# Optimization experiments

Hardware: AMD Instinct MI355X
Metric: run time of the kernel (lower is better)

## Reference

```python
import jax, jax.numpy as jnp
import numpy as np

EMB = 256
HEAD = 8
D = 2 * EMB            # model dim = 512
HD = D // HEAD         # head dim = 64
SCALE = float(np.sqrt(D / HEAD))
NIT = 50               # entmax bisection iterations (entmax lib default)
LN_EPS = 1e-12


def _p(Z, am1):
    # [(alpha-1)x - tau]_+ ** (1/(alpha-1))
    return jnp.maximum(Z, 0.0) ** (1.0 / am1)


def _entmax_impl(X, alpha):
    # X: [B,H,L,L]; alpha: [B,H,L,1], alpha > 1. Faithful port of entmax_bisect.
    am1 = alpha - 1.0
    Xs = X * am1
    d = X.shape[-1]
    max_val = jnp.max(Xs, axis=-1, keepdims=True)
    tau_lo = max_val - 1.0                      # 1 ** (alpha-1)
    tau_hi = max_val - (1.0 / d) ** am1
    f_lo = jnp.sum(_p(Xs - tau_lo, am1), -1, keepdims=True) - 1.0
    dm0 = tau_hi - tau_lo

    def body(i, carry):
        tau_lo, dm, _ = carry
        dm = dm * 0.5
        tau_m = tau_lo + dm
        f_m = jnp.sum(_p(Xs - tau_m, am1), -1, keepdims=True) - 1.0
        tau_lo = jnp.where(f_m * f_lo >= 0, tau_m, tau_lo)
        return (tau_lo, dm, tau_m)

    _, _, tau_m = jax.lax.fori_loop(0, NIT, body, (tau_lo, dm0, tau_lo))
    p = _p(Xs - tau_m, am1)
    return p / jnp.sum(p, -1, keepdims=True)


def entmax_bisect(X, alpha):
    return _entmax_impl(X, alpha)


def reference(X_target_plus, mask, Wq, bq, W1, b1, W2, b2, ln_g, ln_b, Wa, ba):
    X = X_target_plus
    B, L, Dm = X.shape
    # q = dropout(relu(linear_q(x))) ; dropout p=0 -> identity
    q = jax.nn.relu(X @ Wq.T + bq)
    mq = q.reshape(B, L, HEAD, HD).transpose(0, 2, 1, 3)   # [B,H,L,hd]
    mk = X.reshape(B, L, HEAD, HD).transpose(0, 2, 1, 3)   # k = v = X
    scores = jnp.einsum('bhqd,bhkd->bhqk', mq, mk) / SCALE  # [B,H,L,L]
    # mask gets a zero column appended -> last key position always masked
    am = jnp.concatenate([mask, jnp.zeros((B, 1), mask.dtype)], axis=-1)  # [B,L]
    scores = jnp.where(am[:, None, None, :] == 0, -jnp.inf, scores)
    # per-(batch,head) alpha from last query position
    alpha = jax.nn.sigmoid(mq[:, :, -1, :] @ Wa.T + ba) + 1.0   # [B,H,1]
    alpha = jnp.clip(alpha, 1.0 + 1e-5, None)[..., None]        # [B,H,1,1]
    alpha = jnp.broadcast_to(alpha, (B, HEAD, L, 1))
    p = entmax_bisect(scores, alpha)                            # attn dropout p=0
    att = jnp.einsum('bhqk,bhkd->bhqd', p, mk)
    att = att.transpose(0, 2, 1, 3).reshape(B, L, Dm)
    # FFN (dropout p=0) + residual + LayerNorm(eps=1e-12)
    h = jax.nn.relu(att @ W1.T + b1) @ W2.T + b2 + att
    mu = jnp.mean(h, -1, keepdims=True)
    var = jnp.mean((h - mu) ** 2, -1, keepdims=True)
    C_hat = (h - mu) / jnp.sqrt(var + LN_EPS) * ln_g + ln_b
    return C_hat[:, :-1, :], C_hat[:, -1, :]


def setup_inputs() -> dict:
    key = jax.random.key(0)
    ks = jax.random.split(key, 6)
    B, L = 16, 512
    s = 0.02
    return {
        'X_target_plus': jax.random.normal(ks[0], (B, L, D), jnp.float32),
        'mask': jnp.ones((B, L - 1), jnp.float32),
        'Wq': jax.random.normal(ks[1], (D, D), jnp.float32) * s,
        'bq': jnp.zeros((D,), jnp.float32),
        'W1': jax.random.normal(ks[2], (D, D), jnp.float32) * s,
        'b1': jnp.zeros((D,), jnp.float32),
        'W2': jax.random.normal(ks[3], (D, D), jnp.float32) * s,
        'b2': jnp.zeros((D,), jnp.float32),
        'ln_g': jnp.ones((D,), jnp.float32),
        'ln_b': jnp.zeros((D,), jnp.float32),
        'Wa': jax.random.normal(ks[4], (1, HD), jnp.float32) * s,
        'ba': jnp.zeros((1,), jnp.float32),
    }
```

## Files before the change

kernel.cpp:

```cpp
#include <hip/hip_runtime.h>
#include <math.h>

#define BB   16
#define LL   512
#define DD   512
#define HH   8
#define HDIM 64
#define NNEWT 6

typedef unsigned short ushort_t;
typedef __attribute__((ext_vector_type(8))) short short8;
typedef __attribute__((ext_vector_type(4))) float f32x4;

__device__ __forceinline__ float hw_log2(float x) { return __builtin_amdgcn_logf(x); }
__device__ __forceinline__ float hw_exp2(float x) { return __builtin_amdgcn_exp2f(x); }
__device__ __forceinline__ float hw_rcp(float x)  { return __builtin_amdgcn_rcpf(x); }

__device__ __forceinline__ ushort_t f2b(float f) {
    unsigned u = __builtin_bit_cast(unsigned, f);
    unsigned r = u + 0x7FFFu + ((u >> 16) & 1u);
    return (ushort_t)(r >> 16);
}
__device__ __forceinline__ float b2f(ushort_t u) {
    return __builtin_bit_cast(float, ((unsigned)u) << 16);
}

__device__ __forceinline__ float wsum(float v) {
    v += __shfl_xor(v, 1);  v += __shfl_xor(v, 2);  v += __shfl_xor(v, 4);
    v += __shfl_xor(v, 8);  v += __shfl_xor(v, 16); v += __shfl_xor(v, 32);
    return v;
}

template<int CTRL>
__device__ __forceinline__ float dpp_mov(float v) {
    return __builtin_bit_cast(float, __builtin_amdgcn_update_dpp(
        0, __builtin_bit_cast(int, v), CTRL, 0xf, 0xf, true));
}
__device__ __forceinline__ float rsum32(float v) {
    v += dpp_mov<0xB1>(v);
    v += dpp_mov<0x4E>(v);
    v += dpp_mov<0x141>(v);
    v += dpp_mov<0x140>(v);
    v += __shfl_xor(v, 16);
    return v;
}
__device__ __forceinline__ float rmax32(float v) {
    v = fmaxf(v, dpp_mov<0xB1>(v));
    v = fmaxf(v, dpp_mov<0x4E>(v));
    v = fmaxf(v, dpp_mov<0x141>(v));
    v = fmaxf(v, dpp_mov<0x140>(v));
    v = fmaxf(v, __shfl_xor(v, 16));
    return v;
}

#define NEC 4194304
#define WNC 262144
__global__ __launch_bounds__(256) void conv_all(
    const float* __restrict__ X, const float* __restrict__ Wq,
    const float* __restrict__ W1, const float* __restrict__ W2,
    ushort_t* __restrict__ Xb, ushort_t* __restrict__ Wb)
{
    int i = (blockIdx.x * 256 + threadIdx.x) * 4;
    const float* src; ushort_t* dst; int off, doff;
    if (i < NEC) { src = X; dst = Xb; off = i; doff = i; }
    else {
        int k = i - NEC;
        dst = Wb; doff = k;
        if (k < WNC)          { src = Wq; off = k; }
        else if (k < 2 * WNC) { src = W1; off = k - WNC; }
        else                  { src = W2; off = k - 2 * WNC; }
    }
    float4 v = *(const float4*)&src[off];
    ushort4 o;
    o.x = f2b(v.x); o.y = f2b(v.y); o.z = f2b(v.z); o.w = f2b(v.w);
    *(ushort4*)&dst[doff] = o;
}

__device__ __forceinline__ void gload16(const void* g, void* l) {
    __builtin_amdgcn_global_load_lds(
        (const __attribute__((address_space(1))) unsigned*)g,
        (__attribute__((address_space(3))) unsigned*)l, 16, 0, 0);
}

template<int ACT, bool RES, bool OBF16>
__global__ __launch_bounds__(256) void gemm_mfma(
    const ushort_t* __restrict__ A, const ushort_t* __restrict__ W,
    const float* __restrict__ bias, const ushort_t* __restrict__ resid,
    void* __restrict__ Cout, int M, int N, int K)
{
    __shared__ ushort_t Asw[128 * 64];
    __shared__ ushort_t Bsw[64 * 64];

    const int tid = threadIdx.x;
    const int w = tid >> 6, lane = tid & 63;
    const int wm = w >> 1, wn = w & 1;
    const int bm = blockIdx.y * 128, bn = blockIdx.x * 64;

    const int l3 = lane >> 3, l7 = lane & 7;
    const int srcg = l7 ^ l3;
    const int l15 = lane & 15, hi = lane >> 4;

    f32x4 acc[4][2] = {};

    for (int kt = 0; kt < K; kt += 64) {
        #pragma unroll
        for (int u = 0; u < 4; ++u) {
            int q = w * 4 + u;
            gload16(&A[(size_t)(bm + q * 8 + l3) * K + kt + srcg * 8], &Asw[q * 512]);
        }
        #pragma unroll
        for (int u = 0; u < 2; ++u) {
            int q = w * 2 + u;
            gload16(&W[(size_t)(bn + q * 8 + l3) * K + kt + srcg * 8], &Bsw[q * 512]);
        }
        __syncthreads();

        #pragma unroll
        for (int kk = 0; kk < 2; ++kk) {
            const int s = (kk * 4 + hi) ^ l7;
            short8 a[4], b[2];
            #pragma unroll
            for (int f = 0; f < 4; ++f)
                a[f] = *(const short8*)&Asw[(wm * 64 + f * 16 + l15) * 64 + s * 8];
            #pragma unroll
            for (int f = 0; f < 2; ++f)
                b[f] = *(const short8*)&Bsw[(wn * 32 + f * 16 + l15) * 64 + s * 8];
            #pragma unroll
            for (int i = 0; i < 4; ++i)
                #pragma unroll
                for (int j = 0; j < 2; ++j)
                    acc[i][j] = __builtin_amdgcn_mfma_f32_16x16x32_bf16(
                        a[i], b[j], acc[i][j], 0, 0, 0);
        }
        __syncthreads();
    }

    #pragma unroll
    for (int i = 0; i < 4; ++i) {
        #pragma unroll
        for (int j = 0; j < 2; ++j) {
            #pragma unroll
            for (int r = 0; r < 4; ++r) {
                const int m = bm + wm * 64 + i * 16 + hi * 4 + r;
                const int n = bn + wn * 32 + j * 16 + l15;
                float v = acc[i][j][r] + bias[n];
                if (ACT == 1) v = fmaxf(v, 0.f);
                if (RES) v += b2f(resid[(size_t)m * N + n]);
                if (OBF16) ((ushort_t*)Cout)[(size_t)m * N + n] = f2b(v);
                else       ((float*)Cout)[(size_t)m * N + n] = v;
            }
        }
    }
}

__global__ __launch_bounds__(256) void transpose_kt(const ushort_t* __restrict__ Xb,
                                                    ushort_t* __restrict__ Ktb)
{
    int o = blockIdx.x * 256 + threadIdx.x;
    int j = o & 511;
    int d = (o >> 9) & 63;
    int h = (o >> 15) & 7;
    int b = o >> 18;
    Ktb[o] = Xb[((b << 9) + j) * 512 + h * 64 + d];
}

__global__ void alpha_kernel(const ushort_t* __restrict__ Qb, const float* __restrict__ Wa,
                             const float* __restrict__ ba,
                             float* __restrict__ am1v, float* __restrict__ invv)
{
    int t = threadIdx.x;
    if (t >= BB * HH) return;
    int b = t >> 3, h = t & 7;
    float acc = 0.f;
    #pragma unroll
    for (int d = 0; d < HDIM; ++d)
        acc = fmaf(b2f(Qb[((b << 9) + 511) * 512 + h * 64 + d]), Wa[d], acc);
    acc += ba[0];
    float sig = 1.f / (1.f + expf(-acc));
    float alpha = sig + 1.f;
    const float amin = 1.f + 1e-5f;
    if (alpha < amin) alpha = amin;
    float am1 = alpha - 1.f;
    am1v[t] = am1;
    invv[t] = 1.f / am1;
}

#define SLS 520
__global__ __launch_bounds__(256, 4) void attn_kernel(
    const ushort_t* __restrict__ Qb, const ushort_t* __restrict__ Xb,
    const ushort_t* __restrict__ Ktb,
    const float* __restrict__ mask, const float* __restrict__ am1v,
    const float* __restrict__ invv, ushort_t* __restrict__ ATTb)
{
    __shared__ ushort_t qsb[16][72];
    __shared__ float SL[16][SLS];
    __shared__ float attbuf[16][68];

    const int bid = ((blockIdx.x & 7) << 9) + (blockIdx.x >> 3);
    const int bh = bid >> 5;
    const int rg = bid & 31;
    const int b = bh >> 3, h = bh & 7;
    const int tid = threadIdx.x;
    const int w = tid >> 6, lane = tid & 63;
    const int l15 = lane & 15, hi = lane >> 4;

    const float am1 = am1v[bh];
    const float inv = invv[bh];
    const float im1c = fmaxf(inv - 1.f, 1e-30f);
    const float NEG = -__builtin_inff();
    const float sc = 0.125f * am1;
    float* mlds = &attbuf[0][0];

    {
        int idx = tid * 4;
        int rr = idx >> 6, d4 = idx & 63;
        *(ushort4*)&qsb[rr][d4] =
            *(const ushort4*)&Qb[((size_t)((b << 9) + rg * 16 + rr)) * 512 + (h << 6) + d4];
    }
    #pragma unroll
    for (int u = 0; u < 2; ++u) {
        int j = tid + u * 256;
        mlds[j] = (j < 511) ? mask[b * 511 + j] : 0.f;
    }
    __syncthreads();

    {
        const ushort_t* xa = Xb + ((size_t)(b << 9)) * 512 + (h << 6);
        #pragma unroll
        for (int jt = 0; jt < 8; ++jt) {
            const int j0 = w * 128 + jt * 16;
            f32x4 acc = {0.f, 0.f, 0.f, 0.f};
            #pragma unroll
            for (int ks = 0; ks < 2; ++ks) {
                short8 a = *(const short8*)&xa[(size_t)(j0 + l15) * 512 + ks * 32 + hi * 8];
                short8 bf = *(const short8*)&qsb[l15][ks * 32 + hi * 8];
                acc = __builtin_amdgcn_mfma_f32_16x16x32_bf16(a, bf, acc, 0, 0, 0);
            }
            #pragma unroll
            for (int r = 0; r < 4; ++r) {
                int j = j0 + hi * 4 + r;
                float mv = mlds[j];
                SL[l15][j] = (mv == 0.f) ? NEG : acc[r] * sc;
            }
        }
    }
    __syncthreads();

    const int l5 = lane & 31, gg = lane >> 5;
    ushort_t* SLu = (ushort_t*)&SL[0][0];

    #pragma unroll
    for (int pp = 0; pp < 2; ++pp) {
        const int row = w * 4 + pp * 2 + gg;

        float Xs[16];
        #pragma unroll
        for (int u = 0; u < 8; ++u) {
            float2 sv = *(const float2*)&SL[row][u * 64 + 2 * l5];
            Xs[2*u] = sv.x; Xs[2*u+1] = sv.y;
        }

        float mx = Xs[0];
        #pragma unroll
        for (int e = 1; e < 16; ++e) mx = fmaxf(mx, Xs[e]);
        mx = rmax32(mx);

        float tau = mx - 1.f;
        for (int it = 0; it < NNEWT; ++it) {
            float s0 = 0.f, s1 = 0.f, g0 = 0.f, g1 = 0.f;
            #pragma unroll
            for (int e = 0; e < 16; e += 2) {
                float za = fminf(fmaxf(Xs[e]     - tau, 0.f), 1.f);
                float zb = fminf(fmaxf(Xs[e + 1] - tau, 0.f), 1.f);
                float da = hw_exp2(im1c * hw_log2(za));
                float db = hw_exp2(im1c * hw_log2(zb));
                s0 += da * za; g0 += da;
                s1 += db * zb; g1 += db;
            }
            float S  = rsum32(s0 + s1);
            float Sp = rsum32(g0 + g1);
            tau += (S - 1.f) * hw_rcp(inv * Sp);
        }

        float s0 = 0.f, s1 = 0.f;
        #pragma unroll
        for (int u = 0; u < 8; ++u) {
            int j0 = u * 64 + 2 * l5;
            float za = fminf(fmaxf(Xs[2*u]   - tau, 0.f), 1.f);
            float zb = fminf(fmaxf(Xs[2*u+1] - tau, 0.f), 1.f);
            float pa = hw_exp2(inv * hw_log2(za));
            float pb = hw_exp2(inv * hw_log2(zb));
            unsigned pk = (unsigned)f2b(pa) | ((unsigned)f2b(pb) << 16);
            *(unsigned*)&SLu[row * 1040 + j0] = pk;
            s0 += pa; s1 += pb;
        }
        float S = rsum32(s0 + s1);
        if (l5 == 0) SL[row][512] = 1.f / S;
    }
    __syncthreads();

    {
        const ushort_t* ka = Ktb + (size_t)bh * (64 * 512) + (size_t)(w * 16 + l15) * 512;
        const ushort_t* pb = SLu + l15 * 1040;
        f32x4 acc0 = {0.f, 0.f, 0.f, 0.f};
        f32x4 acc1 = {0.f, 0.f, 0.f, 0.f};
        #pragma unroll
        for (int ks = 0; ks < 16; ks += 2) {
            short8 a0 = *(const short8*)&ka[ks * 32 + hi * 8];
            short8 b0 = *(const short8*)&pb[ks * 32 + hi * 8];
            short8 a1 = *(const short8*)&ka[(ks + 1) * 32 + hi * 8];
            short8 b1 = *(const short8*)&pb[(ks + 1) * 32 + hi * 8];
            acc0 = __builtin_amdgcn_mfma_f32_16x16x32_bf16(a0, b0, acc0, 0, 0, 0);
            acc1 = __builtin_amdgcn_mfma_f32_16x16x32_bf16(a1, b1, acc1, 0, 0, 0);
        }
        #pragma unroll
        for (int r = 0; r < 4; ++r)
            attbuf[l15][w * 16 + hi * 4 + r] = acc0[r] + acc1[r];
    }
    __syncthreads();

    {
        int idx = tid * 4;
        int q = idx >> 6, d4 = idx & 63;
        float rn = SL[q][512];
        ushort4 o;
        o.x = f2b(attbuf[q][d4 + 0] * rn);
        o.y = f2b(attbuf[q][d4 + 1] * rn);
        o.z = f2b(attbuf[q][d4 + 2] * rn);
        o.w = f2b(attbuf[q][d4 + 3] * rn);
        *(ushort4*)&ATTb[((size_t)((b << 9) + rg * 16 + q)) * 512 + (h << 6) + d4] = o;
    }
}

__global__ __launch_bounds__(256) void ln_kernel(const float* __restrict__ Cb,
                                                 const float* __restrict__ g,
                                                 const float* __restrict__ beta,
                                                 float* __restrict__ out)
{
    const int w = threadIdx.x >> 6, lane = threadIdx.x & 63;
    const int row = blockIdx.x * 4 + w;
    const int b = row >> 9, l = row & 511;
    const float* x = Cb + (size_t)row * 512;

    float v[8], s = 0.f;
    #pragma unroll
    for (int k = 0; k < 8; ++k) { v[k] = x[k * 64 + lane]; s += v[k]; }
    s = wsum(s);
    float mu = s * (1.f / 512.f);
    float q = 0.f;
    #pragma unroll
    for (int k = 0; k < 8; ++k) { float d = v[k] - mu; q = fmaf(d, d, q); }
    q = wsum(q);
    float rs = rsqrtf(q * (1.f / 512.f) + 1e-12f);

    float* dst = (l < 511) ? (out + (size_t)(b * 511 + l) * 512)
                           : (out + (size_t)16 * 511 * 512 + (size_t)b * 512);
    #pragma unroll
    for (int k = 0; k < 8; ++k) {
        int d = k * 64 + lane;
        dst[d] = (v[k] - mu) * rs * g[d] + beta[d];
    }
}

extern "C" void kernel_launch(void* const* d_in, const int* in_sizes, int n_in,
                              void* d_out, int out_size, void* d_ws, size_t ws_size,
                              hipStream_t stream)
{
    const float* X    = (const float*)d_in[0];
    const float* mask = (const float*)d_in[1];
    const float* Wq   = (const float*)d_in[2];
    const float* bq   = (const float*)d_in[3];
    const float* W1   = (const float*)d_in[4];
    const float* b1   = (const float*)d_in[5];
    const float* W2   = (const float*)d_in[6];
    const float* b2   = (const float*)d_in[7];
    const float* lng  = (const float*)d_in[8];
    const float* lnb  = (const float*)d_in[9];
    const float* Wa   = (const float*)d_in[10];
    const float* ba   = (const float*)d_in[11];
    float* out = (float*)d_out;
    float* ws  = (float*)d_ws;

    const size_t NE = (size_t)BB * LL * DD;
    const size_t WN = (size_t)DD * DD;
    if (ws_size < (3 * NE + 256) * sizeof(float) + 3 * WN * sizeof(ushort_t)) return;

    float* am1v = ws + 3 * NE;
    float* invv = am1v + 128;
    ushort_t* Wqb = (ushort_t*)(am1v + 256);
    ushort_t* W1b = Wqb + WN;
    ushort_t* W2b = W1b + WN;
    ushort_t* Qbb = (ushort_t*)ws;
    ushort_t* Hhb = Qbb + NE;
    ushort_t* ATTb = (ushort_t*)(ws + NE);
    ushort_t* Xb  = (ushort_t*)(ws + 2 * NE);
    ushort_t* Ktb = Xb + NE;
    float* Cb = ws + 2 * NE;

    const int M = BB * LL;

    conv_all<<<(int)((NE + 3 * WN) / 1024), 256, 0, stream>>>(X, Wq, W1, W2, Xb, Wqb);
    gemm_mfma<1, false, true><<<dim3(DD / 64, M / 128), 256, 0, stream>>>(
        Xb, Wqb, bq, nullptr, Qbb, M, DD, DD);
    transpose_kt<<<(int)(NE / 256), 256, 0, stream>>>(Xb, Ktb);
    alpha_kernel<<<1, 128, 0, stream>>>(Qbb, Wa, ba, am1v, invv);
    attn_kernel<<<BB * HH * LL / 16, 256, 0, stream>>>(Qbb, Xb, Ktb, mask, am1v, invv, ATTb);
    gemm_mfma<1, false, true><<<dim3(DD / 64, M / 128), 256, 0, stream>>>(
        ATTb, W1b, b1, nullptr, Hhb, M, DD, DD);
    gemm_mfma<0, true, false><<<dim3(DD / 64, M / 128), 256, 0, stream>>>(
        Hhb, W2b, b2, ATTb, Cb, M, DD, DD);
    ln_kernel<<<M / 4, 256, 0, stream>>>(Cb, lng, lnb, out);
}
```

Baseline: 149.5 us.

## Fuse K transpose into conversion kernel and halve attention rows per block

The separate transpose_kt launch is removed, and the transposed bf16 K is now written by extra blocks of conv_all that read directly from the fp32 input. The attention kernel processes 8 query rows per block instead of 16, doubling the grid and raising the launch-bounds occupancy hint to 8 blocks, with shared memory shrunk to match. Half the MFMA lanes now compute duplicated rows that are discarded, and every block reloads the same K/X tiles, so global read traffic and wasted MFMA work go up in exchange for more parallelism and one fewer launch.

```diff
diff --git a/kernel.cpp b/kernel.cpp
--- a/kernel.cpp
+++ b/kernel.cpp
@@ -58,22 +58,40 @@
 __global__ __launch_bounds__(256) void conv_all(
     const float* __restrict__ X, const float* __restrict__ Wq,
     const float* __restrict__ W1, const float* __restrict__ W2,
-    ushort_t* __restrict__ Xb, ushort_t* __restrict__ Wb)
-{
-    int i = (blockIdx.x * 256 + threadIdx.x) * 4;
-    const float* src; ushort_t* dst; int off, doff;
-    if (i < NEC) { src = X; dst = Xb; off = i; doff = i; }
-    else {
-        int k = i - NEC;
-        dst = Wb; doff = k;
-        if (k < WNC)          { src = Wq; off = k; }
-        else if (k < 2 * WNC) { src = W1; off = k - WNC; }
-        else                  { src = W2; off = k - 2 * WNC; }
-    }
-    float4 v = *(const float4*)&src[off];
-    ushort4 o;
-    o.x = f2b(v.x); o.y = f2b(v.y); o.z = f2b(v.z); o.w = f2b(v.w);
-    *(ushort4*)&dst[doff] = o;
+    ushort_t* __restrict__ Xb, ushort_t* __restrict__ Wb,
+    ushort_t* __restrict__ Ktb)
+{
+    const int SEC1 = NEC / 1024, SEC2 = SEC1 + 3 * WNC / 1024;
+    int blk = blockIdx.x;
+    if (blk < SEC2) {
+        int i = (blk * 256 + threadIdx.x) * 4;
+        const float* src; ushort_t* dst; int off, doff;
+        if (i < NEC) { src = X; dst = Xb; off = i; doff = i; }
+        else {
+            int k = i - NEC;
+            dst = Wb; doff = k;
+            if (k < WNC)          { src = Wq; off = k; }
+            else if (k < 2 * WNC) { src = W1; off = k - WNC; }
+            else                  { src = W2; off = k - 2 * WNC; }
+        }
+        float4 v = *(const float4*)&src[off];
+        ushort4 o;
+        o.x = f2b(v.x); o.y = f2b(v.y); o.z = f2b(v.z); o.w = f2b(v.w);
+        *(ushort4*)&dst[doff] = o;
+    } else {
+        int o = ((blk - SEC2) * 256 + threadIdx.x) * 4;
+        int j = o & 511;
+        int d = (o >> 9) & 63;
+        int h = (o >> 15) & 7;
+        int b = o >> 18;
+        const float* xp = X + ((size_t)(b << 9) + j) * 512 + (h << 6) + d;
+        ushort4 ov;
+        ov.x = f2b(xp[0]);
+        ov.y = f2b(xp[512]);
+        ov.z = f2b(xp[1024]);
+        ov.w = f2b(xp[1536]);
+        *(ushort4*)&Ktb[o] = ov;
+    }
 }
 
 __device__ __forceinline__ void gload16(const void* g, void* l) {
@@ -151,17 +169,6 @@
             }
         }
     }
-}
-
-__global__ __launch_bounds__(256) void transpose_kt(const ushort_t* __restrict__ Xb,
-                                                    ushort_t* __restrict__ Ktb)
-{
-    int o = blockIdx.x * 256 + threadIdx.x;
-    int j = o & 511;
-    int d = (o >> 9) & 63;
-    int h = (o >> 15) & 7;
-    int b = o >> 18;
-    Ktb[o] = Xb[((b << 9) + j) * 512 + h * 64 + d];
 }
 
 __global__ void alpha_kernel(const ushort_t* __restrict__ Qb, const float* __restrict__ Wa,
@@ -186,19 +193,19 @@
 }
 
 #define SLS 520
-__global__ __launch_bounds__(256, 4) void attn_kernel(
+__global__ __launch_bounds__(256, 8) void attn_kernel(
     const ushort_t* __restrict__ Qb, const ushort_t* __restrict__ Xb,
     const ushort_t* __restrict__ Ktb,
     const float* __restrict__ mask, const float* __restrict__ am1v,
     const float* __restrict__ invv, ushort_t* __restrict__ ATTb)
 {
-    __shared__ ushort_t qsb[16][72];
-    __shared__ float SL[16][SLS];
-    __shared__ float attbuf[16][68];
-
-    const int bid = ((blockIdx.x & 7) << 9) + (blockIdx.x >> 3);
-    const int bh = bid >> 5;
-    const int rg = bid & 31;
+    __shared__ ushort_t qsb[8][72];
+    __shared__ float SL[8][SLS];
+    __shared__ float attbuf[8][68];
+
+    const int bid = ((blockIdx.x & 7) << 10) + (blockIdx.x >> 3);
+    const int bh = bid >> 6;
+    const int rg = bid & 63;
     const int b = bh >> 3, h = bh & 7;
     const int tid = threadIdx.x;
     const int w = tid >> 6, lane = tid & 63;
@@ -211,16 +218,16 @@
     const float sc = 0.125f * am1;
     float* mlds = &attbuf[0][0];
 
-    {
+    if (tid < 128) {
         int idx = tid * 4;
         int rr = idx >> 6, d4 = idx & 63;
         *(ushort4*)&qsb[rr][d4] =
-            *(const ushort4*)&Qb[((size_t)((b << 9) + rg * 16 + rr)) * 512 + (h << 6) + d4];
-    }
-    #pragma unroll
-    for (int u = 0; u < 2; ++u) {
-        int j = tid + u * 256;
-        mlds[j] = (j < 511) ? mask[b * 511 + j] : 0.f;
+            *(const ushort4*)&Qb[((size_t)((b << 9) + rg * 8 + rr)) * 512 + (h << 6) + d4];
+    }
+    {
+        mlds[tid] = (tid < 511) ? mask[b * 511 + tid] : 0.f;
+        int j2 = tid + 256;
+        mlds[j2] = (j2 < 511) ? mask[b * 511 + j2] : 0.f;
     }
     __syncthreads();
 
@@ -233,14 +240,16 @@
             #pragma unroll
             for (int ks = 0; ks < 2; ++ks) {
                 short8 a = *(const short8*)&xa[(size_t)(j0 + l15) * 512 + ks * 32 + hi * 8];
-                short8 bf = *(const short8*)&qsb[l15][ks * 32 + hi * 8];
+                short8 bf = *(const short8*)&qsb[l15 & 7][ks * 32 + hi * 8];
                 acc = __builtin_amdgcn_mfma_f32_16x16x32_bf16(a, bf, acc, 0, 0, 0);
             }
-            #pragma unroll
-            for (int r = 0; r < 4; ++r) {
-                int j = j0 + hi * 4 + r;
-                float mv = mlds[j];
-                SL[l15][j] = (mv == 0.f) ? NEG : acc[r] * sc;
+            if (l15 < 8) {
+                #pragma unroll
+                for (int r = 0; r < 4; ++r) {
+                    int j = j0 + hi * 4 + r;
+                    float mv = mlds[j];
+                    SL[l15][j] = (mv == 0.f) ? NEG : acc[r] * sc;
+                }
             }
         }
     }
@@ -248,10 +257,8 @@
 
     const int l5 = lane & 31, gg = lane >> 5;
     ushort_t* SLu = (ushort_t*)&SL[0][0];
-
-    #pragma unroll
-    for (int pp = 0; pp < 2; ++pp) {
-        const int row = w * 4 + pp * 2 + gg;
+    {
+        const int row = w * 2 + gg;
 
         float Xs[16];
         #pragma unroll
@@ -301,7 +308,7 @@
 
     {
         const ushort_t* ka = Ktb + (size_t)bh * (64 * 512) + (size_t)(w * 16 + l15) * 512;
-        const ushort_t* pb = SLu + l15 * 1040;
+        const ushort_t* pb = SLu + (l15 & 7) * 1040;
         f32x4 acc0 = {0.f, 0.f, 0.f, 0.f};
         f32x4 acc1 = {0.f, 0.f, 0.f, 0.f};
         #pragma unroll
@@ -313,22 +320,22 @@
             acc0 = __builtin_amdgcn_mfma_f32_16x16x32_bf16(a0, b0, acc0, 0, 0, 0);
             acc1 = __builtin_amdgcn_mfma_f32_16x16x32_bf16(a1, b1, acc1, 0, 0, 0);
         }
-        #pragma unroll
-        for (int r = 0; r < 4; ++r)
-            attbuf[l15][w * 16 + hi * 4 + r] = acc0[r] + acc1[r];
+        if (l15 < 8) {
+            #pragma unroll
+            for (int r = 0; r < 4; ++r)
+                attbuf[l15][w * 16 + hi * 4 + r] = acc0[r] + acc1[r];
+        }
     }
     __syncthreads();
 
     {
-        int idx = tid * 4;
-        int q = idx >> 6, d4 = idx & 63;
+        int idx = tid * 2;
+        int q = idx >> 6, d2 = idx & 63;
         float rn = SL[q][512];
-        ushort4 o;
-        o.x = f2b(attbuf[q][d4 + 0] * rn);
-        o.y = f2b(attbuf[q][d4 + 1] * rn);
-        o.z = f2b(attbuf[q][d4 + 2] * rn);
-        o.w = f2b(attbuf[q][d4 + 3] * rn);
-        *(ushort4*)&ATTb[((size_t)((b << 9) + rg * 16 + q)) * 512 + (h << 6) + d4] = o;
+        ushort2 o;
+        o.x = f2b(attbuf[q][d2 + 0] * rn);
+        o.y = f2b(attbuf[q][d2 + 1] * rn);
+        *(ushort2*)&ATTb[((size_t)((b << 9) + rg * 8 + q)) * 512 + (h << 6) + d2] = o;
     }
 }
 
@@ -398,13 +405,13 @@
     float* Cb = ws + 2 * NE;
 
     const int M = BB * LL;
-
-    conv_all<<<(int)((NE + 3 * WN) / 1024), 256, 0, stream>>>(X, Wq, W1, W2, Xb, Wqb);
+    const int convBlocks = (int)((NE + 3 * WN) / 1024 + NE / 1024);
+
+    conv_all<<<convBlocks, 256, 0, stream>>>(X, Wq, W1, W2, Xb, Wqb, Ktb);
     gemm_mfma<1, false, true><<<dim3(DD / 64, M / 128), 256, 0, stream>>>(
         Xb, Wqb, bq, nullptr, Qbb, M, DD, DD);
-    transpose_kt<<<(int)(NE / 256), 256, 0, stream>>>(Xb, Ktb);
     alpha_kernel<<<1, 128, 0, stream>>>(Qbb, Wa, ba, am1v, invv);
-    attn_kernel<<<BB * HH * LL / 16, 256, 0, stream>>>(Qbb, Xb, Ktb, mask, am1v, invv, ATTb);
+    attn_kernel<<<BB * HH * LL / 8, 256, 0, stream>>>(Qbb, Xb, Ktb, mask, am1v, invv, ATTb);
     gemm_mfma<1, false, true><<<dim3(DD / 64, M / 128), 256, 0, stream>>>(
         ATTb, W1b, b1, nullptr, Hhb, M, DD, DD);
     gemm_mfma<0, true, false><<<dim3(DD / 64, M / 128), 256, 0, stream>>>(
```

New measurement: 205.7 us. 1.38x slower.
